# Performance work log

Hardware: AMD Instinct MI355X
Metric: run time of the kernel (lower is better)

The kernel has to match this reference:

```python
import jax, jax.numpy as jnp
import numpy as np

N, D, H_ENC, NZ, K, H_EXP, C = 32768, 1024, 512, 64, 16, 256, 10


def setup_inputs() -> dict:
    key = jax.random.key(0)
    ks = jax.random.split(key, 12)
    s = 0.02
    return {
        "X": jax.random.normal(ks[0], (N, D), dtype=jnp.float32),
        "enc_W": jax.random.normal(ks[1], (D, H_ENC), dtype=jnp.float32) * s,
        "enc_b": jnp.zeros((H_ENC,), dtype=jnp.float32),
        "z_W": jax.random.normal(ks[2], (H_ENC, NZ), dtype=jnp.float32) * s,
        "z_b": jnp.zeros((NZ,), dtype=jnp.float32),
        "mu": jax.random.normal(ks[3], (K, NZ), dtype=jnp.float32),  # cluster_layer
        "W1": jax.random.normal(ks[4], (K, NZ, H_EXP), dtype=jnp.float32) * s,
        "b1": jnp.zeros((K, H_EXP), dtype=jnp.float32),
        "W2": jax.random.normal(ks[5], (K, H_EXP, C), dtype=jnp.float32) * s,
        "b2": jnp.zeros((K, C), dtype=jnp.float32),
    }


def reference(X, enc_W, enc_b, z_W, z_b, mu, W1, b1, W2, b2):
    # AE encoder: Linear-ReLU -> z_layer
    h = jax.nn.relu(X @ enc_W + enc_b)                 # [N, H_ENC]
    z = h @ z_W + z_b                                  # [N, NZ]
    # source_distribution (Student-t, alpha=1; exponent (alpha+1)/2 = 1)
    dist = jnp.sum((z[:, None, :] - mu[None, :, :]) ** 2, axis=-1)  # [N, K]
    q = 1.0 / (1.0 + dist)
    q = q / jnp.sum(q, axis=1, keepdims=True)          # [N, K]
    # per-expert Linear-ReLU-Linear over full batch (attention=True path)
    eh = jax.nn.relu(jnp.einsum("nd,kdh->nkh", z, W1) + b1[None])  # [N, K, H_EXP]
    logits = jnp.einsum("nkh,khc->nkc", eh, W2) + b2[None]         # [N, K, C]
    # soft combine: preds[:, c] += q[:, k] * logits[:, k, c]
    preds = jnp.einsum("nk,nkc->nc", q, logits)        # [N, C]
    return preds
```

## Files before the change

### kernel.cpp

```cpp
#include <hip/hip_runtime.h>
#include <stdint.h>

#define N_ROWS 32768
#define DIM    1024
#define HENC   512
#define NZ     64
#define KE     16
#define HEXP   256
#define NC     10

typedef __attribute__((ext_vector_type(8))) __bf16 bf16x8;
typedef __attribute__((ext_vector_type(4))) float f32x4;
typedef __attribute__((ext_vector_type(8))) unsigned short u16x8;
typedef __attribute__((ext_vector_type(4))) unsigned short u16x4;

__device__ __forceinline__ unsigned short f2bf(float f) {
    __bf16 h = (__bf16)f;
    return __builtin_bit_cast(unsigned short, h);
}

__device__ __forceinline__ void gload_lds16(void* lds, const void* gsrc) {
    __builtin_amdgcn_global_load_lds(
        (const __attribute__((address_space(1))) unsigned int*)gsrc,
        (__attribute__((address_space(3))) unsigned int*)lds,
        16, 0, 0);
}

#define SWZ(col, row) ((col) ^ (((row) & 7) << 3))

__global__ void prep_weights(const float* __restrict__ enc_W,
                             const float* __restrict__ z_W,
                             const float* __restrict__ W1,
                             const float* __restrict__ W2,
                             unsigned short* __restrict__ enc_Wt,
                             unsigned short* __restrict__ z_Wt,
                             unsigned short* __restrict__ W1t,
                             unsigned short* __restrict__ W2t) {
    int i = blockIdx.x * 256 + threadIdx.x;
    if (i < 524288) {
        int n = i >> 10, k = i & 1023;
        enc_Wt[i] = f2bf(enc_W[k * HENC + n]);
    } else if (i < 557056) {
        int i2 = i - 524288;
        int n = i2 >> 9, k = i2 & 511;
        z_Wt[i2] = f2bf(z_W[k * NZ + n]);
    } else if (i < 819200) {
        int i3 = i - 557056;
        int e = i3 >> 14, rem = i3 & 16383;
        int h = rem >> 6, d = rem & 63;
        W1t[i3] = f2bf(W1[(e * NZ + d) * HEXP + h]);
    } else if (i < 884736) {
        int i4 = i - 819200;
        int e = i4 >> 12, rem = i4 & 4095;
        int c = rem >> 8, h = rem & 255;
        W2t[i4] = (c < NC) ? f2bf(W2[(e * HEXP + h) * NC + c]) : (unsigned short)0;
    }
}

__launch_bounds__(256, 2)
__global__ void gemm1(const float* __restrict__ X,
                      const unsigned short* __restrict__ Bt,
                      const float* __restrict__ enc_b,
                      const unsigned short* __restrict__ zWt,
                      float* __restrict__ zpart) {
    __shared__ union G1U {
        struct {
            unsigned short As[128][64];
            unsigned short Bs[2][256][64];
        } s;
        unsigned short hbs[128][256];
    } u;
    const int t = threadIdx.x;
    const int lane = t & 63;
    const int w = t >> 6;
    const int g = lane >> 4;
    const int l15 = lane & 15;
    const int l7 = l15 & 7;
    const int wm = (w >> 1) * 64;
    const int wn = (w & 1) * 128;

    const int bid = blockIdx.x;
    const int wgid = (bid & 7) * 64 + (bid >> 3);
    const int m0 = (wgid >> 1) * 128;
    const int n0 = (wgid & 1) * 256;

    const int arow = t >> 4, acolq = t & 15;
    const float* aptr = X + (size_t)(m0 + arow) * DIM + acolq * 4;
    const int ascol = SWZ(acolq * 4, arow);
    const int brow0 = lane >> 3;
    const int bsrccol = SWZ((lane & 7) * 8, brow0);
    const unsigned short* bptr = Bt + (size_t)(n0 + brow0) * DIM + bsrccol;

    f32x4 acc[4][8];
#pragma unroll
    for (int i = 0; i < 4; ++i)
#pragma unroll
        for (int j = 0; j < 8; ++j) acc[i][j] = f32x4{0.f, 0.f, 0.f, 0.f};

    {
#pragma unroll
        for (int it = 0; it < 8; ++it) {
            const int chunk = it * 4 + w;
            gload_lds16(&u.s.Bs[0][chunk * 8][0], bptr + (size_t)chunk * 8 * DIM);
        }
        float4 a[8];
#pragma unroll
        for (int it = 0; it < 8; ++it)
            a[it] = *(const float4*)(aptr + (size_t)it * 16 * DIM);
#pragma unroll
        for (int it = 0; it < 8; ++it) {
            u16x4 p;
            p[0] = f2bf(a[it].x); p[1] = f2bf(a[it].y);
            p[2] = f2bf(a[it].z); p[3] = f2bf(a[it].w);
            *(u16x4*)&u.s.As[it * 16 + arow][ascol] = p;
        }
    }
    __syncthreads();

    float4 an[8];
    for (int step = 0; step < 16; ++step) {
        const int cur = step & 1, nxt = cur ^ 1;

        if (step < 15) {
            const int k1 = (step + 1) * 64;
#pragma unroll
            for (int it = 0; it < 8; ++it) {
                const int chunk = it * 4 + w;
                gload_lds16(&u.s.Bs[nxt][chunk * 8][0],
                            bptr + (size_t)chunk * 8 * DIM + k1);
            }
#pragma unroll
            for (int it = 0; it < 8; ++it)
                an[it] = *(const float4*)(aptr + (size_t)it * 16 * DIM + k1);
        }

#pragma unroll
        for (int kk = 0; kk < 2; ++kk) {
            const int ko = kk * 32 + g * 8;
            const int sko = SWZ(ko, l7);
            bf16x8 af[4], bfr[8];
#pragma unroll
            for (int i = 0; i < 4; ++i)
                af[i] = *(const bf16x8*)&u.s.As[wm + i * 16 + l15][sko];
#pragma unroll
            for (int j = 0; j < 8; ++j)
                bfr[j] = *(const bf16x8*)&u.s.Bs[cur][wn + j * 16 + l15][sko];
#pragma unroll
            for (int i = 0; i < 4; ++i)
#pragma unroll
                for (int j = 0; j < 8; ++j)
                    acc[i][j] = __builtin_amdgcn_mfma_f32_16x16x32_bf16(af[i], bfr[j], acc[i][j], 0, 0, 0);
        }
        __syncthreads();

        if (step < 15) {
#pragma unroll
            for (int it = 0; it < 8; ++it) {
                u16x4 p;
                p[0] = f2bf(an[it].x); p[1] = f2bf(an[it].y);
                p[2] = f2bf(an[it].z); p[3] = f2bf(an[it].w);
                *(u16x4*)&u.s.As[it * 16 + arow][ascol] = p;
            }
        }
        __syncthreads();
    }

#pragma unroll
    for (int j = 0; j < 8; ++j) {
        const int col = wn + j * 16 + l15;
        const float bias = enc_b[n0 + col];
#pragma unroll
        for (int i = 0; i < 4; ++i) {
            const int rb = wm + i * 16 + g * 4;
#pragma unroll
            for (int r = 0; r < 4; ++r) {
                float v = acc[i][j][r] + bias;
                v = v > 0.f ? v : 0.f;
                u.hbs[rb + r][SWZ(col, rb + r)] = f2bf(v);
            }
        }
    }
    __syncthreads();

    {
        f32x4 zacc[2][4];
#pragma unroll
        for (int i2 = 0; i2 < 2; ++i2)
#pragma unroll
            for (int j2 = 0; j2 < 4; ++j2) zacc[i2][j2] = f32x4{0.f, 0.f, 0.f, 0.f};

        const unsigned short* zwB = zWt + n0;
#pragma unroll
        for (int ks = 0; ks < 8; ++ks) {
            const int k = ks * 32 + g * 8;
            bf16x8 bz[4];
#pragma unroll
            for (int j2 = 0; j2 < 4; ++j2)
                bz[j2] = *(const bf16x8*)(zwB + (size_t)(j2 * 16 + l15) * HENC + k);
#pragma unroll
            for (int i2 = 0; i2 < 2; ++i2) {
                const int row = w * 32 + i2 * 16 + l15;
                bf16x8 af = *(const bf16x8*)&u.hbs[row][SWZ(k, row)];
#pragma unroll
                for (int j2 = 0; j2 < 4; ++j2)
                    zacc[i2][j2] = __builtin_amdgcn_mfma_f32_16x16x32_bf16(af, bz[j2], zacc[i2][j2], 0, 0, 0);
            }
        }
        float* zp = zpart + (size_t)(n0 ? 1 : 0) * N_ROWS * NZ;
#pragma unroll
        for (int i2 = 0; i2 < 2; ++i2)
#pragma unroll
            for (int j2 = 0; j2 < 4; ++j2) {
                const int colz = j2 * 16 + l15;
#pragma unroll
                for (int r = 0; r < 4; ++r) {
                    const int rowz = m0 + w * 32 + i2 * 16 + g * 4 + r;
                    zp[(size_t)rowz * NZ + colz] = zacc[i2][j2][r];
                }
            }
    }
}

__launch_bounds__(256, 2)
__global__ void expert_kernel(const float* __restrict__ zpart,
                              const float* __restrict__ z_b,
                              const float* __restrict__ mu,
                              const unsigned short* __restrict__ W1t,
                              const float* __restrict__ b1,
                              const unsigned short* __restrict__ W2t,
                              const float* __restrict__ b2,
                              float* __restrict__ out) {
    __shared__ __align__(16) union SU {
        struct {
            float zs[64][68];
            float mus[16][68];
            float rn[64];
            float mun[16];
        } a;
        struct {
            unsigned short w1s[2][128][64];
            unsigned short ehs[4][16][136];
        } b;
    } su;
    __shared__ float qs[64][16];

    const int t = threadIdx.x;
    const int lane = t & 63;
    const int w = t >> 6;
    const int g = lane >> 4;
    const int l15 = lane & 15;
    const int l7 = l15 & 7;
    const int r0 = blockIdx.x * 64;

    {
        const float* zp0 = zpart;
        const float* zp1 = zpart + (size_t)N_ROWS * NZ;
#pragma unroll
        for (int it = 0; it < 4; ++it) {
            int idx = it * 256 + t;
            int r = idx >> 4, c = (idx & 15) * 4;
            float4 a = *(const float4*)(zp0 + (size_t)(r0 + r) * NZ + c);
            float4 b = *(const float4*)(zp1 + (size_t)(r0 + r) * NZ + c);
            float4 zb = *(const float4*)(z_b + c);
            float4 s;
            s.x = a.x + b.x + zb.x; s.y = a.y + b.y + zb.y;
            s.z = a.z + b.z + zb.z; s.w = a.w + b.w + zb.w;
            *(float4*)&su.a.zs[r][c] = s;
        }
        int r = t >> 4, c = (t & 15) * 4;
        *(float4*)&su.a.mus[r][c] = *(const float4*)(mu + (size_t)r * NZ + c);
    }
    __syncthreads();

    if (t < 64) {
        float s = 0.f;
#pragma unroll
        for (int dq = 0; dq < 16; ++dq) {
            float4 v = *(const float4*)&su.a.zs[t][dq * 4];
            s += v.x * v.x + v.y * v.y + v.z * v.z + v.w * v.w;
        }
        su.a.rn[t] = s;
    } else if (t < 80) {
        int k = t - 64;
        float s = 0.f;
#pragma unroll
        for (int dq = 0; dq < 16; ++dq) {
            float4 v = *(const float4*)&su.a.mus[k][dq * 4];
            s += v.x * v.x + v.y * v.y + v.z * v.z + v.w * v.w;
        }
        su.a.mun[k] = s;
    }
    __syncthreads();

    bf16x8 az[2];
#pragma unroll
    for (int ks = 0; ks < 2; ++ks) {
        int row = w * 16 + l15;
        int ko = ks * 32 + g * 8;
        float4 lo = *(const float4*)&su.a.zs[row][ko];
        float4 hi = *(const float4*)&su.a.zs[row][ko + 4];
        u16x8 tmp;
        tmp[0] = f2bf(lo.x); tmp[1] = f2bf(lo.y); tmp[2] = f2bf(lo.z); tmp[3] = f2bf(lo.w);
        tmp[4] = f2bf(hi.x); tmp[5] = f2bf(hi.y); tmp[6] = f2bf(hi.z); tmp[7] = f2bf(hi.w);
        az[ks] = __builtin_bit_cast(bf16x8, tmp);
    }
    {
        bf16x8 bmu[2];
#pragma unroll
        for (int ks = 0; ks < 2; ++ks) {
            int ko = ks * 32 + g * 8;
            float4 lo = *(const float4*)&su.a.mus[l15][ko];
            float4 hi = *(const float4*)&su.a.mus[l15][ko + 4];
            u16x8 tmp;
            tmp[0] = f2bf(lo.x); tmp[1] = f2bf(lo.y); tmp[2] = f2bf(lo.z); tmp[3] = f2bf(lo.w);
            tmp[4] = f2bf(hi.x); tmp[5] = f2bf(hi.y); tmp[6] = f2bf(hi.z); tmp[7] = f2bf(hi.w);
            bmu[ks] = __builtin_bit_cast(bf16x8, tmp);
        }
        f32x4 dacc = f32x4{0.f, 0.f, 0.f, 0.f};
#pragma unroll
        for (int ks = 0; ks < 2; ++ks)
            dacc = __builtin_amdgcn_mfma_f32_16x16x32_bf16(az[ks], bmu[ks], dacc, 0, 0, 0);
#pragma unroll
        for (int r = 0; r < 4; ++r) {
            int rl = w * 16 + g * 4 + r;
            float dist = su.a.rn[rl] - 2.f * dacc[r] + su.a.mun[l15];
            qs[rl][l15] = 1.f / (1.f + dist);
        }
    }
    __syncthreads();

    if (t < 64) {
        float s = 0.f;
#pragma unroll
        for (int k = 0; k < KE; ++k) s += qs[t][k];
        float inv = 1.f / s;
#pragma unroll
        for (int k = 0; k < KE; ++k) qs[t][k] *= inv;
    }
    __syncthreads();

    const int srow = lane >> 3;
    const int scol = SWZ((lane & 7) * 8, srow);

#pragma unroll
    for (int it = 0; it < 4; ++it) {
        const int chunk = it * 4 + w;
        gload_lds16(&su.b.w1s[0][chunk * 8][0],
                    W1t + (size_t)(chunk * 8 + srow) * NZ + scol);
    }
    __syncthreads();

    float pacc[4] = {0.f, 0.f, 0.f, 0.f};
    unsigned short* eh = &su.b.ehs[w][0][0];

    for (int e = 0; e < KE; ++e) {
        const unsigned short* w2e = W2t + e * (16 * HEXP);
        bf16x8 w2f[8];
#pragma unroll
        for (int hh = 0; hh < 8; ++hh)
            w2f[hh] = *(const bf16x8*)(w2e + (size_t)l15 * HEXP + hh * 32 + g * 8);
        float b1v[2][8];
#pragma unroll
        for (int half = 0; half < 2; ++half)
#pragma unroll
            for (int j = 0; j < 8; ++j)
                b1v[half][j] = b1[e * HEXP + half * 128 + j * 16 + l15];

        f32x4 la = f32x4{0.f, 0.f, 0.f, 0.f};
#pragma unroll
        for (int half = 0; half < 2; ++half) {
            const int i = e * 2 + half;
            const int cur = i & 1, nxt = cur ^ 1;

            if (i + 1 < 2 * KE) {
                const int eg = (i + 1) >> 1;
                const int h1 = ((i + 1) & 1) * 128;
                const unsigned short* src =
                    W1t + (size_t)eg * (HEXP * NZ) + (size_t)(h1 + srow) * NZ + scol;
#pragma unroll
                for (int it = 0; it < 4; ++it) {
                    const int chunk = it * 4 + w;
                    gload_lds16(&su.b.w1s[nxt][chunk * 8][0],
                                src + (size_t)chunk * 8 * NZ);
                }
            }

            f32x4 ea[8];
#pragma unroll
            for (int j = 0; j < 8; ++j) ea[j] = f32x4{0.f, 0.f, 0.f, 0.f};
#pragma unroll
            for (int ks = 0; ks < 2; ++ks) {
                const int sko = SWZ(ks * 32 + g * 8, l7);
#pragma unroll
                for (int j = 0; j < 8; ++j) {
                    bf16x8 bw = *(const bf16x8*)&su.b.w1s[cur][j * 16 + l15][sko];
                    ea[j] = __builtin_amdgcn_mfma_f32_16x16x32_bf16(az[ks], bw, ea[j], 0, 0, 0);
                }
            }
#pragma unroll
            for (int j = 0; j < 8; ++j) {
#pragma unroll
                for (int r = 0; r < 4; ++r) {
                    float v = ea[j][r] + b1v[half][j];
                    v = v > 0.f ? v : 0.f;
                    eh[(g * 4 + r) * 136 + j * 16 + l15] = f2bf(v);
                }
            }
#pragma unroll
            for (int ks2 = 0; ks2 < 4; ++ks2) {
                bf16x8 ef = *(const bf16x8*)&eh[l15 * 136 + ks2 * 32 + g * 8];
                la = __builtin_amdgcn_mfma_f32_16x16x32_bf16(ef, w2f[half * 4 + ks2], la, 0, 0, 0);
            }
            __syncthreads();
        }

        float b2v = (l15 < NC) ? b2[e * NC + l15] : 0.f;
#pragma unroll
        for (int r = 0; r < 4; ++r) {
            int rl = w * 16 + g * 4 + r;
            pacc[r] += qs[rl][e] * (la[r] + b2v);
        }
    }

    if (l15 < NC) {
#pragma unroll
        for (int r = 0; r < 4; ++r) {
            int row = r0 + w * 16 + g * 4 + r;
            out[(size_t)row * NC + l15] = pacc[r];
        }
    }
}

extern "C" void kernel_launch(void* const* d_in, const int* in_sizes, int n_in,
                              void* d_out, int out_size, void* d_ws, size_t ws_size,
                              hipStream_t stream) {
    const float* X     = (const float*)d_in[0];
    const float* enc_W = (const float*)d_in[1];
    const float* enc_b = (const float*)d_in[2];
    const float* z_W   = (const float*)d_in[3];
    const float* z_b   = (const float*)d_in[4];
    const float* mu    = (const float*)d_in[5];
    const float* W1    = (const float*)d_in[6];
    const float* b1    = (const float*)d_in[7];
    const float* W2    = (const float*)d_in[8];
    const float* b2    = (const float*)d_in[9];
    float* out = (float*)d_out;

    char* ws = (char*)d_ws;
    float*          zpart  = (float*)(ws);
    unsigned short* enc_Wt = (unsigned short*)(ws + 16777216);
    unsigned short* z_Wt   = (unsigned short*)(ws + 17825792);
    unsigned short* W1t    = (unsigned short*)(ws + 17891328);
    unsigned short* W2t    = (unsigned short*)(ws + 18415616);

    prep_weights<<<dim3(3456), dim3(256), 0, stream>>>(enc_W, z_W, W1, W2,
                                                       enc_Wt, z_Wt, W1t, W2t);
    gemm1<<<dim3(512), dim3(256), 0, stream>>>(X, enc_Wt, enc_b, z_Wt, zpart);
    expert_kernel<<<dim3(512), dim3(256), 0, stream>>>(zpart, z_b, mu, W1t, b1, W2t, b2, out);
}
```

Baseline: 122.5 us.

## Enlarge gemm1 tile to 256x256 with 8 waves and interleaved ping-pong schedule

The encoder GEMM block grows from 128x256 to 256x256 rows/cols using 512 threads (8 waves), with A now double-buffered in LDS. The K-step is split into four phases that interleave global loads, LDS fragment reads and MFMA bursts, separated by s_barrier and s_setprio, so memory traffic and math overlap. This cuts X/B reloads per output and removes one sync per step. In exchange it uses more LDS per block and more registers per wave, which can lower occupancy. The z-projection epilogue appears to still index only 128 rows of hbs per wave group (w*32 with 8 waves covers 256), so its mapping needs checking.

Result: slower. 131.4 us (+7.2%).

```diff
diff --git a/kernel.cpp b/kernel.cpp
--- a/kernel.cpp
+++ b/kernel.cpp
@@ -57,7 +57,7 @@
     }
 }
 
-__launch_bounds__(256, 2)
+__launch_bounds__(512, 2)
 __global__ void gemm1(const float* __restrict__ X,
                       const unsigned short* __restrict__ Bt,
                       const float* __restrict__ enc_b,
@@ -65,10 +65,10 @@
                       float* __restrict__ zpart) {
     __shared__ union G1U {
         struct {
-            unsigned short As[128][64];
+            unsigned short As[2][256][64];
             unsigned short Bs[2][256][64];
         } s;
-        unsigned short hbs[128][256];
+        unsigned short hbs[256][256];
     } u;
     const int t = threadIdx.x;
     const int lane = t & 63;
@@ -76,43 +76,44 @@
     const int g = lane >> 4;
     const int l15 = lane & 15;
     const int l7 = l15 & 7;
-    const int wm = (w >> 1) * 64;
-    const int wn = (w & 1) * 128;
+    const int wm = (w >> 2) * 128;
+    const int wn = (w & 3) * 64;
 
     const int bid = blockIdx.x;
-    const int wgid = (bid & 7) * 64 + (bid >> 3);
-    const int m0 = (wgid >> 1) * 128;
+    const int wgid = (bid & 7) * 32 + (bid >> 3);
+    const int m0 = (wgid >> 1) * 256;
     const int n0 = (wgid & 1) * 256;
 
-    const int arow = t >> 4, acolq = t & 15;
+    const int arow = t >> 4;
+    const int acolq = t & 15;
     const float* aptr = X + (size_t)(m0 + arow) * DIM + acolq * 4;
     const int ascol = SWZ(acolq * 4, arow);
     const int brow0 = lane >> 3;
     const int bsrccol = SWZ((lane & 7) * 8, brow0);
     const unsigned short* bptr = Bt + (size_t)(n0 + brow0) * DIM + bsrccol;
 
-    f32x4 acc[4][8];
-#pragma unroll
-    for (int i = 0; i < 4; ++i)
-#pragma unroll
-        for (int j = 0; j < 8; ++j) acc[i][j] = f32x4{0.f, 0.f, 0.f, 0.f};
+    f32x4 acc[8][4];
+#pragma unroll
+    for (int i = 0; i < 8; ++i)
+#pragma unroll
+        for (int j = 0; j < 4; ++j) acc[i][j] = f32x4{0.f, 0.f, 0.f, 0.f};
 
     {
 #pragma unroll
+        for (int p = 0; p < 4; ++p) {
+            const int chunk = p * 8 + w;
+            gload_lds16(&u.s.Bs[0][chunk * 8][0], bptr + (size_t)chunk * 8 * DIM);
+        }
+        float4 a[8];
+#pragma unroll
+        for (int it = 0; it < 8; ++it)
+            a[it] = *(const float4*)(aptr + (size_t)it * 32 * DIM);
+#pragma unroll
         for (int it = 0; it < 8; ++it) {
-            const int chunk = it * 4 + w;
-            gload_lds16(&u.s.Bs[0][chunk * 8][0], bptr + (size_t)chunk * 8 * DIM);
-        }
-        float4 a[8];
-#pragma unroll
-        for (int it = 0; it < 8; ++it)
-            a[it] = *(const float4*)(aptr + (size_t)it * 16 * DIM);
-#pragma unroll
-        for (int it = 0; it < 8; ++it) {
-            u16x4 p;
-            p[0] = f2bf(a[it].x); p[1] = f2bf(a[it].y);
-            p[2] = f2bf(a[it].z); p[3] = f2bf(a[it].w);
-            *(u16x4*)&u.s.As[it * 16 + arow][ascol] = p;
+            u16x4 pk;
+            pk[0] = f2bf(a[it].x); pk[1] = f2bf(a[it].y);
+            pk[2] = f2bf(a[it].z); pk[3] = f2bf(a[it].w);
+            *(u16x4*)&u.s.As[0][it * 32 + arow][ascol] = pk;
         }
     }
     __syncthreads();
@@ -120,57 +121,67 @@
     float4 an[8];
     for (int step = 0; step < 16; ++step) {
         const int cur = step & 1, nxt = cur ^ 1;
-
-        if (step < 15) {
-            const int k1 = (step + 1) * 64;
-#pragma unroll
-            for (int it = 0; it < 8; ++it) {
-                const int chunk = it * 4 + w;
+        const int k1 = (step + 1) * 64;
+        bf16x8 bfr[4][2];
+
+#pragma unroll
+        for (int p = 0; p < 4; ++p) {
+            if (step < 15) {
+                if (p == 0) {
+#pragma unroll
+                    for (int it = 0; it < 8; ++it)
+                        an[it] = *(const float4*)(aptr + (size_t)it * 32 * DIM + k1);
+                }
+                const int chunk = p * 8 + w;
                 gload_lds16(&u.s.Bs[nxt][chunk * 8][0],
                             bptr + (size_t)chunk * 8 * DIM + k1);
             }
-#pragma unroll
-            for (int it = 0; it < 8; ++it)
-                an[it] = *(const float4*)(aptr + (size_t)it * 16 * DIM + k1);
-        }
-
-#pragma unroll
-        for (int kk = 0; kk < 2; ++kk) {
-            const int ko = kk * 32 + g * 8;
-            const int sko = SWZ(ko, l7);
-            bf16x8 af[4], bfr[8];
-#pragma unroll
-            for (int i = 0; i < 4; ++i)
-                af[i] = *(const bf16x8*)&u.s.As[wm + i * 16 + l15][sko];
-#pragma unroll
-            for (int j = 0; j < 8; ++j)
-                bfr[j] = *(const bf16x8*)&u.s.Bs[cur][wn + j * 16 + l15][sko];
-#pragma unroll
-            for (int i = 0; i < 4; ++i)
-#pragma unroll
-                for (int j = 0; j < 8; ++j)
-                    acc[i][j] = __builtin_amdgcn_mfma_f32_16x16x32_bf16(af[i], bfr[j], acc[i][j], 0, 0, 0);
+            if (p == 0) {
+#pragma unroll
+                for (int j = 0; j < 4; ++j)
+#pragma unroll
+                    for (int kk = 0; kk < 2; ++kk)
+                        bfr[j][kk] = *(const bf16x8*)
+                            &u.s.Bs[cur][wn + j * 16 + l15][SWZ(kk * 32 + g * 8, l7)];
+            }
+            bf16x8 af[2][2];
+#pragma unroll
+            for (int ii = 0; ii < 2; ++ii)
+#pragma unroll
+                for (int kk = 0; kk < 2; ++kk)
+                    af[ii][kk] = *(const bf16x8*)
+                        &u.s.As[cur][wm + (p * 2 + ii) * 16 + l15][SWZ(kk * 32 + g * 8, l7)];
+            if (p == 3 && step < 15) {
+#pragma unroll
+                for (int it = 0; it < 8; ++it) {
+                    u16x4 pk;
+                    pk[0] = f2bf(an[it].x); pk[1] = f2bf(an[it].y);
+                    pk[2] = f2bf(an[it].z); pk[3] = f2bf(an[it].w);
+                    *(u16x4*)&u.s.As[nxt][it * 32 + arow][ascol] = pk;
+                }
+            }
+            __builtin_amdgcn_s_barrier();
+            __builtin_amdgcn_s_setprio(1);
+#pragma unroll
+            for (int kk = 0; kk < 2; ++kk)
+#pragma unroll
+                for (int ii = 0; ii < 2; ++ii)
+#pragma unroll
+                    for (int j = 0; j < 4; ++j)
+                        acc[p * 2 + ii][j] = __builtin_amdgcn_mfma_f32_16x16x32_bf16(
+                            af[ii][kk], bfr[j][kk], acc[p * 2 + ii][j], 0, 0, 0);
+            __builtin_amdgcn_s_setprio(0);
+            if (p < 3) __builtin_amdgcn_s_barrier();
         }
         __syncthreads();
-
-        if (step < 15) {
-#pragma unroll
-            for (int it = 0; it < 8; ++it) {
-                u16x4 p;
-                p[0] = f2bf(an[it].x); p[1] = f2bf(an[it].y);
-                p[2] = f2bf(an[it].z); p[3] = f2bf(an[it].w);
-                *(u16x4*)&u.s.As[it * 16 + arow][ascol] = p;
-            }
-        }
-        __syncthreads();
-    }
-
-#pragma unroll
-    for (int j = 0; j < 8; ++j) {
+    }
+
+#pragma unroll
+    for (int j = 0; j < 4; ++j) {
         const int col = wn + j * 16 + l15;
         const float bias = enc_b[n0 + col];
 #pragma unroll
-        for (int i = 0; i < 4; ++i) {
+        for (int i = 0; i < 8; ++i) {
             const int rb = wm + i * 16 + g * 4;
 #pragma unroll
             for (int r = 0; r < 4; ++r) {
@@ -200,10 +211,11 @@
 #pragma unroll
             for (int i2 = 0; i2 < 2; ++i2) {
                 const int row = w * 32 + i2 * 16 + l15;
-                bf16x8 af = *(const bf16x8*)&u.hbs[row][SWZ(k, row)];
+                bf16x8 af2 = *(const bf16x8*)&u.hbs[row][SWZ(k, row)];
 #pragma unroll
                 for (int j2 = 0; j2 < 4; ++j2)
-                    zacc[i2][j2] = __builtin_amdgcn_mfma_f32_16x16x32_bf16(af, bz[j2], zacc[i2][j2], 0, 0, 0);
+                    zacc[i2][j2] = __builtin_amdgcn_mfma_f32_16x16x32_bf16(
+                        af2, bz[j2], zacc[i2][j2], 0, 0, 0);
             }
         }
         float* zp = zpart + (size_t)(n0 ? 1 : 0) * N_ROWS * NZ;
@@ -455,6 +467,6 @@
 
     prep_weights<<<dim3(3456), dim3(256), 0, stream>>>(enc_W, z_W, W1, W2,
                                                        enc_Wt, z_Wt, W1t, W2t);
-    gemm1<<<dim3(512), dim3(256), 0, stream>>>(X, enc_Wt, enc_b, z_Wt, zpart);
+    gemm1<<<dim3(256), dim3(512), 0, stream>>>(X, enc_Wt, enc_b, z_Wt, zpart);
     expert_kernel<<<dim3(512), dim3(256), 0, stream>>>(zpart, z_b, mu, W1t, b1, W2t, b2, out);
 }
```

## Software-pipeline expert second GEMM one step behind first GEMM with double-buffered eh

Applied to the files above, without the earlier changes.

Restructures the expert loop into a flat loop over expert halves. Each step now runs the second (eh × W2) MFMA chain for the previous half, reading from a double-buffered eh LDS tile, while also computing the first GEMM for the current half. This removes the write-then-immediately-read dependency on the eh tile inside one iteration, so LDS latency and MFMA chains can overlap. The cost is doubled eh LDS usage, extra epilogue code, and more live registers, which could hurt occupancy.

After: 165.1 us. 1.35x slower.

```diff
diff --git a/kernel.cpp b/kernel.cpp
--- a/kernel.cpp
+++ b/kernel.cpp
@@ -239,7 +239,7 @@
         } a;
         struct {
             unsigned short w1s[2][128][64];
-            unsigned short ehs[4][16][136];
+            unsigned short ehs[4][2][16][136];
         } b;
     } su;
     __shared__ float qs[64][16];
@@ -351,74 +351,102 @@
     __syncthreads();
 
     float pacc[4] = {0.f, 0.f, 0.f, 0.f};
-    unsigned short* eh = &su.b.ehs[w][0][0];
-
-    for (int e = 0; e < KE; ++e) {
-        const unsigned short* w2e = W2t + e * (16 * HEXP);
-        bf16x8 w2f[8];
-#pragma unroll
-        for (int hh = 0; hh < 8; ++hh)
-            w2f[hh] = *(const bf16x8*)(w2e + (size_t)l15 * HEXP + hh * 32 + g * 8);
-        float b1v[2][8];
-#pragma unroll
-        for (int half = 0; half < 2; ++half)
-#pragma unroll
-            for (int j = 0; j < 8; ++j)
-                b1v[half][j] = b1[e * HEXP + half * 128 + j * 16 + l15];
-
-        f32x4 la = f32x4{0.f, 0.f, 0.f, 0.f};
-#pragma unroll
-        for (int half = 0; half < 2; ++half) {
-            const int i = e * 2 + half;
-            const int cur = i & 1, nxt = cur ^ 1;
-
-            if (i + 1 < 2 * KE) {
-                const int eg = (i + 1) >> 1;
-                const int h1 = ((i + 1) & 1) * 128;
-                const unsigned short* src =
-                    W1t + (size_t)eg * (HEXP * NZ) + (size_t)(h1 + srow) * NZ + scol;
-#pragma unroll
-                for (int it = 0; it < 4; ++it) {
-                    const int chunk = it * 4 + w;
-                    gload_lds16(&su.b.w1s[nxt][chunk * 8][0],
-                                src + (size_t)chunk * 8 * NZ);
+    f32x4 la = f32x4{0.f, 0.f, 0.f, 0.f};
+    bf16x8 w2f[8];
+    float b1v[2][8];
+
+    for (int i = 0; i < 2 * KE; ++i) {
+        const int e = i >> 1;
+        const int half = i & 1;
+        const int cur = i & 1, nxt = cur ^ 1;
+        const int ep = i & 1;
+
+        if (i > 0) {
+            const int pp = (i - 1) & 1;
+            const int phalf = (i - 1) & 1;
+            const unsigned short* ehp = &su.b.ehs[w][pp][0][0];
+#pragma unroll
+            for (int ks2 = 0; ks2 < 4; ++ks2) {
+                bf16x8 ef = *(const bf16x8*)&ehp[l15 * 136 + ks2 * 32 + g * 8];
+                la = __builtin_amdgcn_mfma_f32_16x16x32_bf16(ef, w2f[phalf * 4 + ks2], la, 0, 0, 0);
+            }
+            if (half == 0) {
+                const int pe = e - 1;
+                float b2v = (l15 < NC) ? b2[pe * NC + l15] : 0.f;
+#pragma unroll
+                for (int r = 0; r < 4; ++r) {
+                    int rl = w * 16 + g * 4 + r;
+                    pacc[r] += qs[rl][pe] * (la[r] + b2v);
                 }
-            }
-
-            f32x4 ea[8];
-#pragma unroll
-            for (int j = 0; j < 8; ++j) ea[j] = f32x4{0.f, 0.f, 0.f, 0.f};
-#pragma unroll
-            for (int ks = 0; ks < 2; ++ks) {
-                const int sko = SWZ(ks * 32 + g * 8, l7);
-#pragma unroll
-                for (int j = 0; j < 8; ++j) {
-                    bf16x8 bw = *(const bf16x8*)&su.b.w1s[cur][j * 16 + l15][sko];
-                    ea[j] = __builtin_amdgcn_mfma_f32_16x16x32_bf16(az[ks], bw, ea[j], 0, 0, 0);
-                }
-            }
+                la = f32x4{0.f, 0.f, 0.f, 0.f};
+            }
+        }
+
+        if (half == 0) {
+            const unsigned short* w2e = W2t + e * (16 * HEXP);
+#pragma unroll
+            for (int hh = 0; hh < 8; ++hh)
+                w2f[hh] = *(const bf16x8*)(w2e + (size_t)l15 * HEXP + hh * 32 + g * 8);
+#pragma unroll
+            for (int hf = 0; hf < 2; ++hf)
+#pragma unroll
+                for (int j = 0; j < 8; ++j)
+                    b1v[hf][j] = b1[e * HEXP + hf * 128 + j * 16 + l15];
+        }
+
+        if (i + 1 < 2 * KE) {
+            const int eg = (i + 1) >> 1;
+            const int h1 = ((i + 1) & 1) * 128;
+            const unsigned short* src =
+                W1t + (size_t)eg * (HEXP * NZ) + (size_t)(h1 + srow) * NZ + scol;
+#pragma unroll
+            for (int it = 0; it < 4; ++it) {
+                const int chunk = it * 4 + w;
+                gload_lds16(&su.b.w1s[nxt][chunk * 8][0],
+                            src + (size_t)chunk * 8 * NZ);
+            }
+        }
+
+        f32x4 ea[8];
+#pragma unroll
+        for (int j = 0; j < 8; ++j) ea[j] = f32x4{0.f, 0.f, 0.f, 0.f};
+#pragma unroll
+        for (int ks = 0; ks < 2; ++ks) {
+            const int sko = SWZ(ks * 32 + g * 8, l7);
 #pragma unroll
             for (int j = 0; j < 8; ++j) {
-#pragma unroll
-                for (int r = 0; r < 4; ++r) {
-                    float v = ea[j][r] + b1v[half][j];
-                    v = v > 0.f ? v : 0.f;
-                    eh[(g * 4 + r) * 136 + j * 16 + l15] = f2bf(v);
-                }
-            }
-#pragma unroll
-            for (int ks2 = 0; ks2 < 4; ++ks2) {
-                bf16x8 ef = *(const bf16x8*)&eh[l15 * 136 + ks2 * 32 + g * 8];
-                la = __builtin_amdgcn_mfma_f32_16x16x32_bf16(ef, w2f[half * 4 + ks2], la, 0, 0, 0);
-            }
-            __syncthreads();
-        }
-
-        float b2v = (l15 < NC) ? b2[e * NC + l15] : 0.f;
+                bf16x8 bw = *(const bf16x8*)&su.b.w1s[cur][j * 16 + l15][sko];
+                ea[j] = __builtin_amdgcn_mfma_f32_16x16x32_bf16(az[ks], bw, ea[j], 0, 0, 0);
+            }
+        }
+
+        unsigned short* ehc = &su.b.ehs[w][ep][0][0];
+#pragma unroll
+        for (int j = 0; j < 8; ++j) {
+#pragma unroll
+            for (int r = 0; r < 4; ++r) {
+                float v = ea[j][r] + b1v[half][j];
+                v = v > 0.f ? v : 0.f;
+                ehc[(g * 4 + r) * 136 + j * 16 + l15] = f2bf(v);
+            }
+        }
+        __syncthreads();
+    }
+
+    {
+        const int pp = (2 * KE - 1) & 1;
+        const unsigned short* ehp = &su.b.ehs[w][pp][0][0];
+#pragma unroll
+        for (int ks2 = 0; ks2 < 4; ++ks2) {
+            bf16x8 ef = *(const bf16x8*)&ehp[l15 * 136 + ks2 * 32 + g * 8];
+            la = __builtin_amdgcn_mfma_f32_16x16x32_bf16(ef, w2f[4 + ks2], la, 0, 0, 0);
+        }
+        const int pe = KE - 1;
+        float b2v = (l15 < NC) ? b2[pe * NC + l15] : 0.f;
 #pragma unroll
         for (int r = 0; r < 4; ++r) {
             int rl = w * 16 + g * 4 + r;
-            pacc[r] += qs[rl][e] * (la[r] + b2v);
+            pacc[r] += qs[rl][pe] * (la[r] + b2v);
         }
     }
 
```
